# Performance work log

Measured on AMD Instinct MI355X. Metric: run time of the kernel, lower is better.

Reference implementation:

```python
import jax, jax.numpy as jnp
import numpy as np

S, B, H, L = 512, 32, 512, 2
P = 0.2  # recurrent_dropout


def setup_inputs() -> dict:
    key = jax.random.key(0)
    ks = jax.random.split(key, 8)
    sc = 0.05
    x = jax.random.normal(ks[0], (S, B, H), dtype=jnp.float32)
    # per-token keep mask, broadcast over hidden dim
    mask = (jax.random.uniform(ks[1], (S, B, 1)) < 0.9).astype(jnp.float32)
    W_ih = jax.random.normal(ks[2], (L, 4 * H, H), dtype=jnp.float32) * sc
    b_ih = jnp.zeros((L, 4 * H), jnp.float32)
    W_hh = jax.random.normal(ks[3], (L, 4 * H, H), dtype=jnp.float32) * sc
    b_hh = jnp.zeros((L, 4 * H), jnp.float32)
    Wg_in = jax.random.normal(ks[4], (L, H, H), dtype=jnp.float32) * sc
    bg_in = jnp.zeros((L, H), jnp.float32)
    # highway_gate_state is the SAME Linear shared across layers ([module]*L aliasing)
    Wg_state = jax.random.normal(ks[5], (H, H), dtype=jnp.float32) * sc
    bg_state = jnp.zeros((H,), jnp.float32)
    Wl_in = jax.random.normal(ks[6], (L, H, H), dtype=jnp.float32) * sc
    # fixed recurrent dropout mask (fix_mask=True, Train=True), inverted-dropout scaling
    drop_mask = (jax.random.uniform(ks[7], (L, B, H)) > P).astype(jnp.float32) / (1.0 - P)
    return {"x": x, "mask": mask, "W_ih": W_ih, "b_ih": b_ih, "W_hh": W_hh,
            "b_hh": b_hh, "Wg_in": Wg_in, "bg_in": bg_in, "Wg_state": Wg_state,
            "bg_state": bg_state, "Wl_in": Wl_in, "drop_mask": drop_mask, "Train": 1}


def _run(x, mask, W_ih, b_ih, W_hh, b_hh, Wg_in, bg_in, Wg_state, bg_state, Wl_in, drop_mask, train):
    for l in range(L):
        Wih, bih, Whh, bhh = W_ih[l], b_ih[l], W_hh[l], b_hh[l]
        Wgi, bgi, Wli, dm = Wg_in[l], bg_in[l], Wl_in[l], drop_mask[l]

        def step(carry, xm):
            h, c = carry
            xt, mt = xm  # xt: [B, H], mt: [B, 1]
            gates = xt @ Wih.T + bih + h @ Whh.T + bhh  # [B, 4H]
            i, f, g, o = jnp.split(gates, 4, axis=-1)   # PyTorch LSTMCell order i,f,g,o
            c_t = jax.nn.sigmoid(f) * c + jax.nn.sigmoid(i) * jnp.tanh(g)
            h_t = jax.nn.sigmoid(o) * jnp.tanh(c_t)
            r = jax.nn.sigmoid(xt @ Wgi.T + bgi + h @ Wg_state.T + bg_state)
            h_t = r * h_t + (1.0 - r) * (xt @ Wli.T)
            if train:
                h_t = dm * h_t
            h = mt * h_t + (1.0 - mt) * h
            c = mt * c_t + (1.0 - mt) * c
            return (h, c), h

        h0 = jnp.zeros((x.shape[1], H), x.dtype)
        _, outs = jax.lax.scan(step, (h0, h0), (x, mask))
        # DeepLSTM.flip along time before next layer
        x = outs[::-1]
        mask = mask[::-1]
    # output_state = flipped last-layer outputs, transposed to [batch, seq, hidden]
    return jnp.transpose(x, (1, 0, 2))


def reference(x, mask, W_ih, b_ih, W_hh, b_hh, Wg_in, bg_in, Wg_state, bg_state, Wl_in, drop_mask, Train):
    return _run(x, mask, W_ih, b_ih, W_hh, b_hh, Wg_in, bg_in, Wg_state, bg_state,
                Wl_in, drop_mask, bool(Train))
```

## Files before the change

### kernel.cpp

```cpp
#include <hip/hip_runtime.h>
#include <math.h>

#define SEQ 512
#define BAT 32
#define HID 512
#define NG  3072
#define CH  32
#define NB  32
#define UPB 16
#define DSTR 81
#define HOSTR 20
#define PASTR 72

typedef __attribute__((ext_vector_type(8))) short bfrag;
typedef __attribute__((ext_vector_type(4))) float f32x4;
typedef unsigned long long u64;

__device__ __forceinline__ float sigf(float x) { return 1.f / (1.f + expf(-x)); }

__device__ __forceinline__ unsigned short f2bf(float x) {
    unsigned u = __float_as_uint(x);
    return (unsigned short)((u + 0x7fffu + ((u >> 16) & 1u)) >> 16);
}
__device__ __forceinline__ unsigned pk2(float a, float b) {
    return (unsigned)f2bf(a) | ((unsigned)f2bf(b) << 16);
}

__global__ __launch_bounds__(256) void proj_gemm(
    const float* __restrict__ xin, int t0, int rev,
    const float* __restrict__ Wih, const float* __restrict__ Wgi,
    const float* __restrict__ Wli,
    const float* __restrict__ bih, const float* __restrict__ bhh,
    const float* __restrict__ bgi, const float* __restrict__ bgs,
    float* __restrict__ Pt)
{
    __shared__ unsigned short As[64 * PASTR];
    __shared__ unsigned short Bs[64 * PASTR];

    const int tid = threadIdx.x;
    const int bm = blockIdx.x;
    const int bn = blockIdx.y;
    const int lane = tid & 63, wv = tid >> 6;
    const int row15 = lane & 15, koff8 = (lane >> 4) * 8;

    f32x4 acc[4];
#pragma unroll
    for (int i = 0; i < 4; i++) acc[i] = (f32x4){0.f, 0.f, 0.f, 0.f};

    const int r = tid >> 2, q = tid & 3;
    const int gm = bm * 64 + r;
    const int tt = t0 + (gm >> 5), bb = gm & 31;
    const int pt = rev ? (SEQ - 1 - tt) : tt;
    const float* arow = xin + ((size_t)pt * BAT + bb) * HID;
    const int gn = bn * 64 + r;
    const float* brow = (gn < 2048) ? (Wih + (size_t)gn * HID)
                      : (gn < 2560) ? (Wgi + (size_t)(gn - 2048) * HID)
                                    : (Wli + (size_t)(gn - 2560) * HID);

    for (int k0 = 0; k0 < HID; k0 += 64) {
        {
            const float* ap = arow + k0 + q * 16;
            float4 v0 = ((const float4*)ap)[0];
            float4 v1 = ((const float4*)ap)[1];
            float4 v2 = ((const float4*)ap)[2];
            float4 v3 = ((const float4*)ap)[3];
            uint4 w0 = { pk2(v0.x,v0.y), pk2(v0.z,v0.w), pk2(v1.x,v1.y), pk2(v1.z,v1.w) };
            uint4 w1 = { pk2(v2.x,v2.y), pk2(v2.z,v2.w), pk2(v3.x,v3.y), pk2(v3.z,v3.w) };
            *(uint4*)&As[r * PASTR + q * 16]     = w0;
            *(uint4*)&As[r * PASTR + q * 16 + 8] = w1;
            const float* bp = brow + k0 + q * 16;
            v0 = ((const float4*)bp)[0];
            v1 = ((const float4*)bp)[1];
            v2 = ((const float4*)bp)[2];
            v3 = ((const float4*)bp)[3];
            uint4 x0 = { pk2(v0.x,v0.y), pk2(v0.z,v0.w), pk2(v1.x,v1.y), pk2(v1.z,v1.w) };
            uint4 x1 = { pk2(v2.x,v2.y), pk2(v2.z,v2.w), pk2(v3.x,v3.y), pk2(v3.z,v3.w) };
            *(uint4*)&Bs[r * PASTR + q * 16]     = x0;
            *(uint4*)&Bs[r * PASTR + q * 16 + 8] = x1;
        }
        __syncthreads();
        const unsigned short* ha = &As[(wv * 16 + row15) * PASTR + koff8];
#pragma unroll
        for (int ks = 0; ks < 2; ks++) {
            bfrag a = *(const bfrag*)(ha + ks * 32);
#pragma unroll
            for (int nt = 0; nt < 4; nt++) {
                bfrag bf = *(const bfrag*)(&Bs[(nt * 16 + row15) * PASTR + koff8 + ks * 32]);
                acc[nt] = __builtin_amdgcn_mfma_f32_16x16x32_bf16(a, bf, acc[nt], 0, 0, 0);
            }
        }
        __syncthreads();
    }

    const int ml = wv * 16 + (lane >> 4) * 4;
    const int gm2 = bm * 64 + ml;
    const int tl = gm2 >> 5, b0 = gm2 & 31;
#pragma unroll
    for (int nt = 0; nt < 4; nt++) {
        int gn2 = bn * 64 + nt * 16 + row15;
        float bias = (gn2 < 2048) ? (bih[gn2] + bhh[gn2])
                   : (gn2 < 2560) ? (bgi[gn2 - 2048] + bgs[gn2 - 2048])
                                  : 0.f;
        float4 o = { acc[nt][0] + bias, acc[nt][1] + bias,
                     acc[nt][2] + bias, acc[nt][3] + bias };
        *(float4*)&Pt[((size_t)tl * NG + gn2) * BAT + b0] = o;
    }
}

#define GLD(J, OFF) \
    asm volatile("global_load_dwordx2 %0, %1, off offset:" #OFF " sc0 sc1" \
                 : "=v"(v[J]) : "v"(srcb));
#define GATHER16 \
    GLD(0,0)     GLD(1,256)   GLD(2,512)   GLD(3,768) \
    GLD(4,1024)  GLD(5,1280)  GLD(6,1536)  GLD(7,1792) \
    GLD(8,2048)  GLD(9,2304)  GLD(10,2560) GLD(11,2816) \
    GLD(12,3072) GLD(13,3328) GLD(14,3584) GLD(15,3840)
#define VMWAIT \
    asm volatile("s_waitcnt vmcnt(0)" ::: "memory"); \
    __builtin_amdgcn_sched_barrier(0);

__global__ __launch_bounds__(512, 1) void scan_chunk(
    const float* __restrict__ Pt,
    const float* __restrict__ Whh,
    const float* __restrict__ Wgs,
    u64* __restrict__ Htag,
    float* __restrict__ Hf32,
    float* __restrict__ Cbuf,
    const float* __restrict__ mask,
    const float* __restrict__ dm,
    float* __restrict__ Y,
    float* __restrict__ out,
    int l, int c,
    const int* __restrict__ trainPtr)
{
    __shared__ uint4 h16[16 * 4 * 32];
    __shared__ float Dst[BAT * DSTR];
    __shared__ float hout[BAT * HOSTR];

    const int tid = threadIdx.x;
    const int u0 = blockIdx.x * UPB;
    const int b = tid & 31;
    const int ul = tid >> 5;
    const int lane = tid & 63;
    const int wv = tid >> 6;
    const int rev = (l == 1);
    const int row15 = lane & 15;
    const int koff = (lane >> 4) * 8;

    const int mtA = wv / 5, ntA = wv % 5;
    const int has2 = (wv < 2);
    const int mtB = 1, ntB = 3 + wv;

    bfrag wA[16], wB[16];
    {
        const float* rA = (ntA < 4) ? (Whh + ((size_t)(ntA * 512 + u0 + row15)) * 512)
                                    : (Wgs + (size_t)(u0 + row15) * 512);
#pragma unroll
        for (int ks = 0; ks < 16; ks++) {
            int k = koff + ks * 32;
            float4 x0 = *(const float4*)(rA + k);
            float4 x1 = *(const float4*)(rA + k + 4);
            bfrag f;
            f[0] = (short)f2bf(x0.x); f[1] = (short)f2bf(x0.y);
            f[2] = (short)f2bf(x0.z); f[3] = (short)f2bf(x0.w);
            f[4] = (short)f2bf(x1.x); f[5] = (short)f2bf(x1.y);
            f[6] = (short)f2bf(x1.z); f[7] = (short)f2bf(x1.w);
            wA[ks] = f;
        }
        if (has2) {
            const float* rB = (ntB < 4) ? (Whh + ((size_t)(ntB * 512 + u0 + row15)) * 512)
                                        : (Wgs + (size_t)(u0 + row15) * 512);
#pragma unroll
            for (int ks = 0; ks < 16; ks++) {
                int k = koff + ks * 32;
                float4 x0 = *(const float4*)(rB + k);
                float4 x1 = *(const float4*)(rB + k + 4);
                bfrag f;
                f[0] = (short)f2bf(x0.x); f[1] = (short)f2bf(x0.y);
                f[2] = (short)f2bf(x0.z); f[3] = (short)f2bf(x0.w);
                f[4] = (short)f2bf(x1.x); f[5] = (short)f2bf(x1.y);
                f[6] = (short)f2bf(x1.z); f[7] = (short)f2bf(x1.w);
                wB[ks] = f;
            }
        } else {
#pragma unroll
            for (int ks = 0; ks < 16; ks++) wB[ks] = wA[ks];
        }
    }

    const int u = u0 + ul;
    float h = Hf32[b * HID + u];
    float cc = Cbuf[b * HID + u];
    const int train = *trainPtr;
    const float dmv = train ? dm[b * HID + u] : 1.0f;

    const char* hb = (const char*)h16;
    const char* haA = hb + (size_t)(lane >> 4) * 512 + (mtA * 16 + row15) * 16;
    const char* haB = hb + (size_t)(lane >> 4) * 512 + (mtB * 16 + row15) * 16;

    for (int s = 0; s < CH; s++) {
        const int t = c * CH + s;
        const int par = t & 1;
        const int tPhys = rev ? (SEQ - 1 - t) : t;

        {
            const u64* srcb = Htag + (size_t)par * 8192 + (size_t)ul * 512 + b;
            u64 v[16];
            GATHER16
            VMWAIT
            const unsigned ex = (unsigned)t;
            while (true) {
                unsigned bad = 0;
#pragma unroll
                for (int j = 0; j < 16; j++)
                    bad |= ((unsigned)(v[j] >> 32)) ^ ex;
                if (!bad) break;
                GATHER16
                VMWAIT
            }
#pragma unroll
            for (int q = 0; q < 4; q++) {
                uint4 wq;
                wq.x = (unsigned)v[4 * q + 0];
                wq.y = (unsigned)v[4 * q + 1];
                wq.z = (unsigned)v[4 * q + 2];
                wq.w = (unsigned)v[4 * q + 3];
                h16[(ul * 4 + q) * 32 + b] = wq;
            }
        }

        const float* Pb = Pt + (size_t)s * NG * BAT;
        float pi = Pb[(size_t)(0 * HID + u) * BAT + b];
        float pf = Pb[(size_t)(1 * HID + u) * BAT + b];
        float pg = Pb[(size_t)(2 * HID + u) * BAT + b];
        float po = Pb[(size_t)(3 * HID + u) * BAT + b];
        float pr = Pb[(size_t)(4 * HID + u) * BAT + b];
        float xl = Pb[(size_t)(5 * HID + u) * BAT + b];
        float mk = mask[(size_t)tPhys * BAT + b];
        __syncthreads();

        {
            f32x4 acA = {0.f, 0.f, 0.f, 0.f};
            f32x4 acB = {0.f, 0.f, 0.f, 0.f};
#pragma unroll
            for (int ks = 0; ks < 16; ks++) {
                acA = __builtin_amdgcn_mfma_f32_16x16x32_bf16(
                        *(const bfrag*)(haA + (size_t)ks * 2048), wA[ks], acA, 0, 0, 0);
                if (has2)
                    acB = __builtin_amdgcn_mfma_f32_16x16x32_bf16(
                        *(const bfrag*)(haB + (size_t)ks * 2048), wB[ks], acB, 0, 0, 0);
            }
            int mrA = mtA * 16 + (lane >> 4) * 4, clA = ntA * 16 + row15;
#pragma unroll
            for (int r = 0; r < 4; r++) Dst[(mrA + r) * DSTR + clA] = acA[r];
            if (has2) {
                int mrB = mtB * 16 + (lane >> 4) * 4, clB = ntB * 16 + row15;
#pragma unroll
                for (int r = 0; r < 4; r++) Dst[(mrB + r) * DSTR + clB] = acB[r];
            }
        }
        __syncthreads();

        float gi = sigf(pi + Dst[b * DSTR + 0  + ul]);
        float gf = sigf(pf + Dst[b * DSTR + 16 + ul]);
        float gg = tanhf(pg + Dst[b * DSTR + 32 + ul]);
        float go = sigf(po + Dst[b * DSTR + 48 + ul]);
        float gr = sigf(pr + Dst[b * DSTR + 64 + ul]);
        float ct = gf * cc + gi * gg;
        float hr_ = go * tanhf(ct);
        float h2 = (gr * hr_ + (1.f - gr) * xl) * dmv;
        float hn = mk * h2 + (1.f - mk) * h;
        cc = mk * ct + (1.f - mk) * cc;
        h = hn;

        {
            unsigned mybf = (unsigned)f2bf(hn);
            unsigned part = __shfl_xor(mybf, 32, 64);
            if (lane < 32) {
                u64 pv = (u64)(mybf | (part << 16)) | ((u64)(unsigned)(t + 1) << 32);
                u64* dst = Htag + (size_t)(par ^ 1) * 8192
                                + ((size_t)(blockIdx.x * 8 + wv)) * 32 + b;
                asm volatile("global_store_dwordx2 %0, %1, off sc0 sc1"
                             :: "v"(dst), "v"(pv) : "memory");
            }
        }

        hout[b * HOSTR + ul] = hn;
        __syncthreads();
        if (tid < 128) {
            int bb = tid >> 2, q = tid & 3;
            float4 o = *(const float4*)&hout[bb * HOSTR + 4 * q];
            if (l == 0)
                *(float4*)&Y[(size_t)t * BAT * HID + bb * HID + u0 + 4 * q] = o;
            else
                *(float4*)&out[(size_t)bb * SEQ * HID
                               + (size_t)(SEQ - 1 - t) * HID + u0 + 4 * q] = o;
        }
    }

    Hf32[b * HID + u] = h;
    Cbuf[b * HID + u] = cc;
}

extern "C" void kernel_launch(void* const* d_in, const int* in_sizes, int n_in,
                              void* d_out, int out_size, void* d_ws, size_t ws_size,
                              hipStream_t stream) {
    const float* x        = (const float*)d_in[0];
    const float* mask     = (const float*)d_in[1];
    const float* W_ih     = (const float*)d_in[2];
    const float* b_ih     = (const float*)d_in[3];
    const float* W_hh     = (const float*)d_in[4];
    const float* b_hh     = (const float*)d_in[5];
    const float* Wg_in    = (const float*)d_in[6];
    const float* bg_in    = (const float*)d_in[7];
    const float* Wg_state = (const float*)d_in[8];
    const float* bg_state = (const float*)d_in[9];
    const float* Wl_in    = (const float*)d_in[10];
    const float* drop     = (const float*)d_in[11];
    const int*   train    = (const int*)d_in[12];
    float* out = (float*)d_out;

    float* Pt   = (float*)d_ws;
    float* Y    = Pt + (size_t)CH * NG * BAT;
    u64*   Htag = (u64*)(Y + (size_t)SEQ * BAT * HID);
    float* Hf32 = (float*)(Htag + 2 * 8192);
    float* Cbuf = Hf32 + BAT * HID;

    for (int l = 0; l < 2; l++) {
        const int rev = l;
        const float* Wih = W_ih + (size_t)l * 4 * HID * HID;
        const float* Whh = W_hh + (size_t)l * 4 * HID * HID;
        const float* Wgi = Wg_in + (size_t)l * HID * HID;
        const float* Wli = Wl_in + (size_t)l * HID * HID;
        const float* bih = b_ih + (size_t)l * 4 * HID;
        const float* bhh = b_hh + (size_t)l * 4 * HID;
        const float* bgi = bg_in + (size_t)l * HID;
        const float* dm  = drop + (size_t)l * BAT * HID;
        const float* xin = l ? Y : x;

        hipMemsetAsync(Htag, 0,
                       (size_t)2 * 8192 * 8 + (size_t)2 * BAT * HID * 4,
                       stream);

        for (int c = 0; c < SEQ / CH; c++) {
            proj_gemm<<<dim3((CH * BAT) / 64, NG / 64), 256, 0, stream>>>(
                xin, c * CH, rev, Wih, Wgi, Wli, bih, bhh, bgi, bg_state, Pt);
            scan_chunk<<<NB, 512, 0, stream>>>(
                Pt, Whh, Wg_state, Htag, Hf32, Cbuf, mask, dm, Y, out,
                l, c, train);
        }
    }
}
```

Measured before the change: 4.854 ms.

## Overlap next-chunk input projection with recurrent scan in one launch using bf16 buffers

The input projection for chunk c+1 now runs inside the same launch as the scan for chunk c, on extra blocks beyond the 32 scan blocks, writing into a double-buffered projection workspace. The projection output is stored as bf16 instead of fp32 to halve its traffic. The spin-wait now re-polls only stale entries with atomic loads and a sleep, the recurrent MFMA loop is split into two accumulator chains, and the h store is issued before the state update. This costs extra launch width, competition between projection and scan blocks for CUs and bandwidth, and some precision loss in the projected gates.

```diff
diff --git a/kernel.cpp b/kernel.cpp
--- a/kernel.cpp
+++ b/kernel.cpp
@@ -11,6 +11,7 @@
 #define DSTR 81
 #define HOSTR 20
 #define PASTR 72
+#define NPROJB 192
 
 typedef __attribute__((ext_vector_type(8))) short bfrag;
 typedef __attribute__((ext_vector_type(4))) float f32x4;
@@ -25,21 +26,20 @@
 __device__ __forceinline__ unsigned pk2(float a, float b) {
     return (unsigned)f2bf(a) | ((unsigned)f2bf(b) << 16);
 }
-
-__global__ __launch_bounds__(256) void proj_gemm(
-    const float* __restrict__ xin, int t0, int rev,
+__device__ __forceinline__ float bf2f(unsigned short s) {
+    return __uint_as_float((unsigned)s << 16);
+}
+
+__device__ __forceinline__ void proj_tile(
+    int jd, const float* __restrict__ xin, int t0, int rev,
     const float* __restrict__ Wih, const float* __restrict__ Wgi,
     const float* __restrict__ Wli,
     const float* __restrict__ bih, const float* __restrict__ bhh,
     const float* __restrict__ bgi, const float* __restrict__ bgs,
-    float* __restrict__ Pt)
+    unsigned short* __restrict__ Pt,
+    unsigned short* As, unsigned short* Bs, int tid)
 {
-    __shared__ unsigned short As[64 * PASTR];
-    __shared__ unsigned short Bs[64 * PASTR];
-
-    const int tid = threadIdx.x;
-    const int bm = blockIdx.x;
-    const int bn = blockIdx.y;
+    const int bm = jd & 7, bn = jd >> 3;
     const int lane = tid & 63, wv = tid >> 6;
     const int row15 = lane & 15, koff8 = (lane >> 4) * 8;
 
@@ -48,14 +48,18 @@
     for (int i = 0; i < 4; i++) acc[i] = (f32x4){0.f, 0.f, 0.f, 0.f};
 
     const int r = tid >> 2, q = tid & 3;
-    const int gm = bm * 64 + r;
+    const int gm = bm * 128 + r;
     const int tt = t0 + (gm >> 5), bb = gm & 31;
     const int pt = rev ? (SEQ - 1 - tt) : tt;
     const float* arow = xin + ((size_t)pt * BAT + bb) * HID;
-    const int gn = bn * 64 + r;
-    const float* brow = (gn < 2048) ? (Wih + (size_t)gn * HID)
-                      : (gn < 2560) ? (Wgi + (size_t)(gn - 2048) * HID)
-                                    : (Wli + (size_t)(gn - 2560) * HID);
+
+    const float* brow = nullptr;
+    if (tid < 256) {
+        const int gn = bn * 64 + r;
+        brow = (gn < 2048) ? (Wih + (size_t)gn * HID)
+             : (gn < 2560) ? (Wgi + (size_t)(gn - 2048) * HID)
+                           : (Wli + (size_t)(gn - 2560) * HID);
+    }
 
     for (int k0 = 0; k0 < HID; k0 += 64) {
         {
@@ -68,15 +72,17 @@
             uint4 w1 = { pk2(v2.x,v2.y), pk2(v2.z,v2.w), pk2(v3.x,v3.y), pk2(v3.z,v3.w) };
             *(uint4*)&As[r * PASTR + q * 16]     = w0;
             *(uint4*)&As[r * PASTR + q * 16 + 8] = w1;
-            const float* bp = brow + k0 + q * 16;
-            v0 = ((const float4*)bp)[0];
-            v1 = ((const float4*)bp)[1];
-            v2 = ((const float4*)bp)[2];
-            v3 = ((const float4*)bp)[3];
-            uint4 x0 = { pk2(v0.x,v0.y), pk2(v0.z,v0.w), pk2(v1.x,v1.y), pk2(v1.z,v1.w) };
-            uint4 x1 = { pk2(v2.x,v2.y), pk2(v2.z,v2.w), pk2(v3.x,v3.y), pk2(v3.z,v3.w) };
-            *(uint4*)&Bs[r * PASTR + q * 16]     = x0;
-            *(uint4*)&Bs[r * PASTR + q * 16 + 8] = x1;
+            if (tid < 256) {
+                const float* bp = brow + k0 + q * 16;
+                v0 = ((const float4*)bp)[0];
+                v1 = ((const float4*)bp)[1];
+                v2 = ((const float4*)bp)[2];
+                v3 = ((const float4*)bp)[3];
+                uint4 x0 = { pk2(v0.x,v0.y), pk2(v0.z,v0.w), pk2(v1.x,v1.y), pk2(v1.z,v1.w) };
+                uint4 x1 = { pk2(v2.x,v2.y), pk2(v2.z,v2.w), pk2(v3.x,v3.y), pk2(v3.z,v3.w) };
+                *(uint4*)&Bs[r * PASTR + q * 16]     = x0;
+                *(uint4*)&Bs[r * PASTR + q * 16 + 8] = x1;
+            }
         }
         __syncthreads();
         const unsigned short* ha = &As[(wv * 16 + row15) * PASTR + koff8];
@@ -92,8 +98,8 @@
         __syncthreads();
     }
 
-    const int ml = wv * 16 + (lane >> 4) * 4;
-    const int gm2 = bm * 64 + ml;
+    const int ml = wv * 16 + ((lane >> 4) << 2);
+    const int gm2 = bm * 128 + ml;
     const int tl = gm2 >> 5, b0 = gm2 & 31;
 #pragma unroll
     for (int nt = 0; nt < 4; nt++) {
@@ -101,10 +107,24 @@
         float bias = (gn2 < 2048) ? (bih[gn2] + bhh[gn2])
                    : (gn2 < 2560) ? (bgi[gn2 - 2048] + bgs[gn2 - 2048])
                                   : 0.f;
-        float4 o = { acc[nt][0] + bias, acc[nt][1] + bias,
-                     acc[nt][2] + bias, acc[nt][3] + bias };
-        *(float4*)&Pt[((size_t)tl * NG + gn2) * BAT + b0] = o;
-    }
+        uint2 o = { pk2(acc[nt][0] + bias, acc[nt][1] + bias),
+                    pk2(acc[nt][2] + bias, acc[nt][3] + bias) };
+        *(uint2*)&Pt[((size_t)tl * NG + gn2) * BAT + b0] = o;
+    }
+}
+
+__global__ __launch_bounds__(512) void proj_gemm(
+    const float* __restrict__ xin, int t0, int rev,
+    const float* __restrict__ Wih, const float* __restrict__ Wgi,
+    const float* __restrict__ Wli,
+    const float* __restrict__ bih, const float* __restrict__ bhh,
+    const float* __restrict__ bgi, const float* __restrict__ bgs,
+    unsigned short* __restrict__ Pt)
+{
+    __shared__ unsigned short As[128 * PASTR];
+    __shared__ unsigned short Bs[64 * PASTR];
+    proj_tile(blockIdx.x, xin, t0, rev, Wih, Wgi, Wli, bih, bhh, bgi, bgs,
+              Pt, As, Bs, threadIdx.x);
 }
 
 #define GLD(J, OFF) \
@@ -120,7 +140,7 @@
     __builtin_amdgcn_sched_barrier(0);
 
 __global__ __launch_bounds__(512, 1) void scan_chunk(
-    const float* __restrict__ Pt,
+    const unsigned short* __restrict__ PtR,
     const float* __restrict__ Whh,
     const float* __restrict__ Wgs,
     u64* __restrict__ Htag,
@@ -131,19 +151,39 @@
     float* __restrict__ Y,
     float* __restrict__ out,
     int l, int c,
-    const int* __restrict__ trainPtr)
+    const int* __restrict__ trainPtr,
+    const float* __restrict__ xin, int do_proj,
+    const float* __restrict__ Wih, const float* __restrict__ Wgi,
+    const float* __restrict__ Wli,
+    const float* __restrict__ bih, const float* __restrict__ bhh,
+    const float* __restrict__ bgi, const float* __restrict__ bgs,
+    unsigned short* __restrict__ PtW)
 {
     __shared__ uint4 h16[16 * 4 * 32];
     __shared__ float Dst[BAT * DSTR];
     __shared__ float hout[BAT * HOSTR];
+    __shared__ unsigned short As[128 * PASTR];
+    __shared__ unsigned short Bs[64 * PASTR];
 
     const int tid = threadIdx.x;
+    const int rev = (l == 1);
+
+    if (blockIdx.x >= NB) {
+        if (do_proj) {
+            int j0 = ((int)blockIdx.x - NB) * 2;
+            proj_tile(j0, xin, (c + 1) * CH, rev, Wih, Wgi, Wli,
+                      bih, bhh, bgi, bgs, PtW, As, Bs, tid);
+            proj_tile(j0 + 1, xin, (c + 1) * CH, rev, Wih, Wgi, Wli,
+                      bih, bhh, bgi, bgs, PtW, As, Bs, tid);
+        }
+        return;
+    }
+
     const int u0 = blockIdx.x * UPB;
     const int b = tid & 31;
     const int ul = tid >> 5;
     const int lane = tid & 63;
     const int wv = tid >> 6;
-    const int rev = (l == 1);
     const int row15 = lane & 15;
     const int koff = (lane >> 4) * 8;
 
@@ -203,20 +243,25 @@
         const int par = t & 1;
         const int tPhys = rev ? (SEQ - 1 - t) : t;
 
+        const u64* srcb = Htag + (size_t)par * 8192 + (size_t)ul * 512 + b;
+        u64 v[16];
         {
-            const u64* srcb = Htag + (size_t)par * 8192 + (size_t)ul * 512 + b;
-            u64 v[16];
             GATHER16
             VMWAIT
             const unsigned ex = (unsigned)t;
-            while (true) {
-                unsigned bad = 0;
+            unsigned bad = 0;
+#pragma unroll
+            for (int j = 0; j < 16; j++) bad |= ((unsigned)(v[j] >> 32)) ^ ex;
+            while (bad) {
+                __builtin_amdgcn_s_sleep(1);
 #pragma unroll
                 for (int j = 0; j < 16; j++)
-                    bad |= ((unsigned)(v[j] >> 32)) ^ ex;
-                if (!bad) break;
-                GATHER16
-                VMWAIT
+                    if (((unsigned)(v[j] >> 32)) != ex)
+                        v[j] = __hip_atomic_load(srcb + (size_t)j * 32,
+                                                 __ATOMIC_RELAXED, __HIP_MEMORY_SCOPE_AGENT);
+                bad = 0;
+#pragma unroll
+                for (int j = 0; j < 16; j++) bad |= ((unsigned)(v[j] >> 32)) ^ ex;
             }
 #pragma unroll
             for (int q = 0; q < 4; q++) {
@@ -229,31 +274,38 @@
             }
         }
 
-        const float* Pb = Pt + (size_t)s * NG * BAT;
-        float pi = Pb[(size_t)(0 * HID + u) * BAT + b];
-        float pf = Pb[(size_t)(1 * HID + u) * BAT + b];
-        float pg = Pb[(size_t)(2 * HID + u) * BAT + b];
-        float po = Pb[(size_t)(3 * HID + u) * BAT + b];
-        float pr = Pb[(size_t)(4 * HID + u) * BAT + b];
-        float xl = Pb[(size_t)(5 * HID + u) * BAT + b];
+        const unsigned short* Pb = PtR + (size_t)s * NG * BAT;
+        float pi = bf2f(Pb[(size_t)(0 * HID + u) * BAT + b]);
+        float pf = bf2f(Pb[(size_t)(1 * HID + u) * BAT + b]);
+        float pg = bf2f(Pb[(size_t)(2 * HID + u) * BAT + b]);
+        float po = bf2f(Pb[(size_t)(3 * HID + u) * BAT + b]);
+        float pr = bf2f(Pb[(size_t)(4 * HID + u) * BAT + b]);
+        float xl = bf2f(Pb[(size_t)(5 * HID + u) * BAT + b]);
         float mk = mask[(size_t)tPhys * BAT + b];
         __syncthreads();
 
         {
-            f32x4 acA = {0.f, 0.f, 0.f, 0.f};
-            f32x4 acB = {0.f, 0.f, 0.f, 0.f};
-#pragma unroll
-            for (int ks = 0; ks < 16; ks++) {
-                acA = __builtin_amdgcn_mfma_f32_16x16x32_bf16(
-                        *(const bfrag*)(haA + (size_t)ks * 2048), wA[ks], acA, 0, 0, 0);
-                if (has2)
-                    acB = __builtin_amdgcn_mfma_f32_16x16x32_bf16(
-                        *(const bfrag*)(haB + (size_t)ks * 2048), wB[ks], acB, 0, 0, 0);
-            }
+            f32x4 aA0 = {0.f,0.f,0.f,0.f}, aA1 = {0.f,0.f,0.f,0.f};
+            f32x4 aB0 = {0.f,0.f,0.f,0.f}, aB1 = {0.f,0.f,0.f,0.f};
+#pragma unroll
+            for (int ks = 0; ks < 8; ks++) {
+                aA0 = __builtin_amdgcn_mfma_f32_16x16x32_bf16(
+                        *(const bfrag*)(haA + (size_t)ks * 2048), wA[ks], aA0, 0, 0, 0);
+                aA1 = __builtin_amdgcn_mfma_f32_16x16x32_bf16(
+                        *(const bfrag*)(haA + (size_t)(ks + 8) * 2048), wA[ks + 8], aA1, 0, 0, 0);
+                if (has2) {
+                    aB0 = __builtin_amdgcn_mfma_f32_16x16x32_bf16(
+                            *(const bfrag*)(haB + (size_t)ks * 2048), wB[ks], aB0, 0, 0, 0);
+                    aB1 = __builtin_amdgcn_mfma_f32_16x16x32_bf16(
+                            *(const bfrag*)(haB + (size_t)(ks + 8) * 2048), wB[ks + 8], aB1, 0, 0, 0);
+                }
+            }
+            f32x4 acA = aA0 + aA1;
             int mrA = mtA * 16 + (lane >> 4) * 4, clA = ntA * 16 + row15;
 #pragma unroll
             for (int r = 0; r < 4; r++) Dst[(mrA + r) * DSTR + clA] = acA[r];
             if (has2) {
+                f32x4 acB = aB0 + aB1;
                 int mrB = mtB * 16 + (lane >> 4) * 4, clB = ntB * 16 + row15;
 #pragma unroll
                 for (int r = 0; r < 4; r++) Dst[(mrB + r) * DSTR + clB] = acB[r];
@@ -270,8 +322,6 @@
         float hr_ = go * tanhf(ct);
         float h2 = (gr * hr_ + (1.f - gr) * xl) * dmv;
         float hn = mk * h2 + (1.f - mk) * h;
-        cc = mk * ct + (1.f - mk) * cc;
-        h = hn;
 
         {
             unsigned mybf = (unsigned)f2bf(hn);
@@ -284,6 +334,8 @@
                              :: "v"(dst), "v"(pv) : "memory");
             }
         }
+        cc = mk * ct + (1.f - mk) * cc;
+        h = hn;
 
         hout[b * HOSTR + ul] = hn;
         __syncthreads();
@@ -320,8 +372,9 @@
     const int*   train    = (const int*)d_in[12];
     float* out = (float*)d_out;
 
-    float* Pt   = (float*)d_ws;
-    float* Y    = Pt + (size_t)CH * NG * BAT;
+    unsigned short* Pt0 = (unsigned short*)d_ws;
+    unsigned short* Pt1 = Pt0 + (size_t)CH * NG * BAT;
+    float* Y    = (float*)(Pt1 + (size_t)CH * NG * BAT);
     u64*   Htag = (u64*)(Y + (size_t)SEQ * BAT * HID);
     float* Hf32 = (float*)(Htag + 2 * 8192);
     float* Cbuf = Hf32 + BAT * HID;
@@ -342,12 +395,17 @@
                        (size_t)2 * 8192 * 8 + (size_t)2 * BAT * HID * 4,
                        stream);
 
+        proj_gemm<<<384, 512, 0, stream>>>(
+            xin, 0, rev, Wih, Wgi, Wli, bih, bhh, bgi, bg_state, Pt0);
+
         for (int c = 0; c < SEQ / CH; c++) {
-            proj_gemm<<<dim3((CH * BAT) / 64, NG / 64), 256, 0, stream>>>(
-                xin, c * CH, rev, Wih, Wgi, Wli, bih, bhh, bgi, bg_state, Pt);
-            scan_chunk<<<NB, 512, 0, stream>>>(
-                Pt, Whh, Wg_state, Htag, Hf32, Cbuf, mask, dm, Y, out,
-                l, c, train);
-        }
-    }
-}
+            unsigned short* PtR = (c & 1) ? Pt1 : Pt0;
+            unsigned short* PtW = (c & 1) ? Pt0 : Pt1;
+            scan_chunk<<<NB + NPROJB, 512, 0, stream>>>(
+                PtR, Whh, Wg_state, Htag, Hf32, Cbuf, mask, dm, Y, out,
+                l, c, train,
+                xin, (c < SEQ / CH - 1) ? 1 : 0,
+                Wih, Wgi, Wli, bih, bhh, bgi, bg_state, PtW);
+        }
+    }
+}
```

Measured after the change: 3.986 ms. 1.22x faster.
